# Kernel optimization log

Hardware: AMD Instinct MI355X
Metric: run time of the kernel (lower is better)

## Reference

```python
import jax, jax.numpy as jnp
import numpy as np

GROUP_SIZE = 128
NIBBLES = 8  # int4 values packed per int32


def dequantize(qweight, qzeros, scales):
    """Unpack int4 weights/zeros and dequantize: w = (q - z) * scale.

    qweight: [in/8, out] int32, 8 int4 values packed along the IN dim.
    qzeros:  [groups, out/8] int32, 8 int4 zeros packed along the OUT dim.
    scales:  [groups, out] fp16.
    Returns w: [in, out] fp16.
    """
    shifts = (jnp.arange(NIBBLES, dtype=jnp.int32) * 4)
    # unpack weights along input dim -> [in/8, 8, out] -> [in, out]
    q = ((qweight[:, None, :] >> shifts[None, :, None]) & 15)
    q = q.reshape(-1, qweight.shape[1])
    # unpack zeros along output dim -> [groups, out/8, 8] -> [groups, out]
    z = ((qzeros[:, :, None] >> shifts[None, None, :]) & 15)
    z = z.reshape(qzeros.shape[0], -1)
    # broadcast per-group zeros/scales to per-input-row
    z_full = jnp.repeat(z, GROUP_SIZE, axis=0).astype(scales.dtype)   # [in, out]
    s_full = jnp.repeat(scales, GROUP_SIZE, axis=0)                    # [in, out]
    return (q.astype(scales.dtype) - z_full) * s_full


def setup_inputs() -> dict:
    key = jax.random.key(0)
    k1, k2, k3, k4, k5 = jax.random.split(key, 5)
    B, S, IN, OUT, G = 2, 2048, 4096, 11008, 32
    x = jax.random.normal(k1, (B, S, IN), dtype=jnp.float16)
    qweight = jax.random.randint(k2, (IN // 8, OUT), 0, 2147483647, dtype=jnp.int32)
    qzeros = jax.random.randint(k3, (G, OUT // 8), 0, 2147483647, dtype=jnp.int32)
    scales = jax.random.uniform(k4, (G, OUT), dtype=jnp.float16, minval=0.001, maxval=0.02)
    bias = jax.random.normal(k5, (OUT,), dtype=jnp.float16)
    return {"x": x, "qweight": qweight, "qzeros": qzeros, "scales": scales, "bias": bias}


def reference(x, qweight, qzeros, scales, bias):
    w = dequantize(qweight, qzeros, scales)  # [in, out] fp16
    # q4_matmul accumulates in fp32, emits fp16
    out = jnp.einsum('bsi,io->bso', x, w, preferred_element_type=jnp.float32)
    out = out.astype(jnp.float16) + bias
    return out
```

## Files before the change

kernel.cpp:

```cpp
#include <hip/hip_runtime.h>
#include <cstdint>
#include <cstddef>


typedef unsigned short u16;
typedef u16    u16x8  __attribute__((ext_vector_type(8)));
typedef __bf16 bfv8   __attribute__((ext_vector_type(8)));
typedef float  f32x4  __attribute__((ext_vector_type(4)));

#define K_DIM 4096
#define N_DIM 11008
#define GS    128
#define KT64  (K_DIM / 64)
#define LSTR  72

__device__ __forceinline__ u16 f2bf(float f) {
  union { float f; uint32_t u; } v;
  v.f = f;
  uint32_t u = v.u + 0x7FFFu + ((v.u >> 16) & 1u);
  return (u16)(u >> 16);
}
__device__ __forceinline__ float f16r(float v) {
  return (float)(_Float16)v;
}
__device__ __forceinline__ void async_load16(const u16* g, u16* l) {
  __builtin_amdgcn_global_load_lds(
      (const __attribute__((address_space(1))) uint32_t*)g,
      (__attribute__((address_space(3))) uint32_t*)l, 16, 0, 0);
}

__global__ __launch_bounds__(256) void convert_x_tiled(
    const float* __restrict__ x, u16* __restrict__ xb) {
  const int kt = blockIdx.x, mt = blockIdx.y;
  const int k0 = kt * 64, m0 = mt * 128;
  u16* dst = xb + ((size_t)(mt * KT64 + kt)) * 8192;
#pragma unroll
  for (int i = 0; i < 4; ++i) {
    const int g  = i * 256 + threadIdx.x;
    const int nl = g >> 3;
    const int cg = (g & 7) ^ (nl & 7);
    const float* sp = x + (size_t)(m0 + nl) * K_DIM + (k0 + cg * 8);
    const f32x4 p = *(const f32x4*)sp;
    const f32x4 q = *(const f32x4*)(sp + 4);
    u16x8 o;
#pragma unroll
    for (int t = 0; t < 4; ++t) { o[t] = f2bf(p[t]); o[t + 4] = f2bf(q[t]); }
    *(u16x8*)(dst + (size_t)g * 8) = o;
  }
}

__global__ __launch_bounds__(256) void dequant_tiled(
    const uint32_t* __restrict__ qweight, const uint32_t* __restrict__ qzeros,
    const float* __restrict__ scales, u16* __restrict__ wt) {
  const int kt = blockIdx.x, nt = blockIdx.y;
  const int n0 = nt * 128;
  const int gq = kt >> 1;
  u16* dst = wt + ((size_t)(nt * KT64 + kt)) * 8192;
#pragma unroll
  for (int i = 0; i < 4; ++i) {
    const int g  = i * 256 + threadIdx.x;
    const int nl = g >> 3;
    const int cg = (g & 7) ^ (nl & 7);
    const int n  = n0 + nl;
    const uint32_t zq = qzeros[(size_t)gq * (N_DIM / 8) + (n >> 3)];
    const int   z   = (int)((zq >> ((n & 7) * 4)) & 15u);
    const float s   = scales[(size_t)gq * N_DIM + n];
    const float nzs = -s * (float)z;
    const uint32_t q = qweight[(size_t)(kt * 8 + cg) * N_DIM + n];
    u16x8 o;
#pragma unroll
    for (int t = 0; t < 8; ++t) {
      const int qv = (int)((q >> (t * 4)) & 15u);
      o[t] = f2bf(fmaf((float)qv, s, nzs));
    }
    *(u16x8*)(dst + (size_t)g * 8) = o;
  }
}

#define LDF(p) __builtin_bit_cast(bfv8, *(const u16x8*)(p))
#define BAR()  asm volatile("s_barrier" ::: "memory")
#define VMW(n) asm volatile("s_waitcnt vmcnt(" #n ")" ::: "memory")

#define STAGE_AH(ktt, h) do {                                                 \
    const u16* s_ = at0 + ((size_t)(h) * KT64 + (ktt)) * 8192;                \
    u16* d_ = &As[(((ktt) & 1) * 16384) + (h) * 8192 + wave * 512];           \
    async_load16(s_ + (size_t)tid * 8, d_);                                   \
    async_load16(s_ + (size_t)(512 + tid) * 8, d_ + 4096);                    \
  } while (0)
#define STAGE_BH(ktt, h) do {                                                 \
    const u16* s_ = bt0 + ((size_t)(h) * KT64 + (ktt)) * 8192;                \
    u16* d_ = &Bs[(((ktt) & 1) * 16384) + (h) * 8192 + wave * 512];           \
    async_load16(s_ + (size_t)tid * 8, d_);                                   \
    async_load16(s_ + (size_t)(512 + tid) * 8, d_ + 4096);                    \
  } while (0)

#define RD_AP(v, ib, sbx) do {                                                \
    v[0] = LDF(&As[(sbx) * 16384 + aoff + (ib) * 1024 + kq0]);                \
    v[1] = LDF(&As[(sbx) * 16384 + aoff + (ib) * 1024 + kq1]);                \
    v[2] = LDF(&As[(sbx) * 16384 + aoff + ((ib) + 1) * 1024 + kq0]);          \
    v[3] = LDF(&As[(sbx) * 16384 + aoff + ((ib) + 1) * 1024 + kq1]);          \
  } while (0)
#define RD_B8(v, sbx) do {                                                    \
    _Pragma("unroll")                                                         \
    for (int j_ = 0; j_ < 4; ++j_) {                                          \
      v[2 * j_]     = LDF(&Bs[(sbx) * 16384 + boff + j_ * 1024 + kq0]);       \
      v[2 * j_ + 1] = LDF(&Bs[(sbx) * 16384 + boff + j_ * 1024 + kq1]);       \
    }                                                                         \
  } while (0)

#define MM(ib, av, bv) do {                                                   \
    __builtin_amdgcn_s_setprio(1);                                            \
    _Pragma("unroll")                                                         \
    for (int ks_ = 0; ks_ < 2; ++ks_)                                         \
      _Pragma("unroll")                                                       \
      for (int ii_ = 0; ii_ < 2; ++ii_)                                       \
        _Pragma("unroll")                                                     \
        for (int j_ = 0; j_ < 4; ++j_)                                        \
          acc[(ib) + ii_][j_] = __builtin_amdgcn_mfma_f32_16x16x32_bf16(      \
              av[2 * ii_ + ks_], bv[2 * j_ + ks_], acc[(ib) + ii_][j_],       \
              0, 0, 0);                                                       \
    __builtin_amdgcn_s_setprio(0);                                            \
  } while (0)

#define KTILE_BODY(kt, sb, bcur, bnxt) do {                                   \
    RD_AP(a23, 2, sb);  STAGE_AH((kt) + 1, 0);  MM(0, a01, bcur);  BAR();     \
    RD_AP(a45, 4, sb);  STAGE_AH((kt) + 1, 1);  MM(2, a23, bcur);  BAR();     \
    RD_AP(a67, 6, sb);  STAGE_BH((kt) + 2, 0);  MM(4, a45, bcur);             \
    VMW(2);  BAR();                                                           \
    RD_B8(bnxt, (sb) ^ 1);  RD_AP(a01, 0, (sb) ^ 1);  STAGE_BH((kt) + 2, 1);  \
    MM(6, a67, bcur);  BAR();                                                 \
  } while (0)

__global__ __launch_bounds__(512, 2) void gemm_256(
    const u16* __restrict__ xb, const u16* __restrict__ wt,
    const float* __restrict__ bias, float* __restrict__ out) {
  __shared__ __align__(16) u16 As[2 * 16384];
  __shared__ __align__(16) u16 Bs[2 * 16384];

  const int tid  = threadIdx.x;
  const int lane = tid & 63;
  const int wave = tid >> 6;
  const int wm   = wave >> 2;
  const int wn   = wave & 3;
  const int lrow = lane & 15;
  const int lk   = lane >> 4;
  const int swz  = lrow & 7;

  const int nwg = gridDim.x * gridDim.y;
  int wg = blockIdx.y * gridDim.x + blockIdx.x;
  if ((nwg & 7) == 0) wg = (wg & 7) * (nwg >> 3) + (wg >> 3);
  const int bx = wg % gridDim.x;
  const int by = wg / gridDim.x;
  const int n0 = bx * 256;
  const int m0 = by * 256;

  const u16* at0 = xb + (size_t)(2 * by) * KT64 * 8192;
  const u16* bt0 = wt + (size_t)(2 * bx) * KT64 * 8192;

  const int aoff = wm * 8192 + lrow * 64;
  const int boff = (wn >> 1) * 8192 + ((wn & 1) * 64 + lrow) * 64;
  const int kq0  = (lk ^ swz) * 8;
  const int kq1  = ((4 + lk) ^ swz) * 8;

  bfv8 a01[4], a23[4], a45[4], a67[4], bA[8], bB[8];
  f32x4 acc[8][4];
#pragma unroll
  for (int i = 0; i < 8; ++i)
#pragma unroll
    for (int j = 0; j < 4; ++j) acc[i][j] = f32x4{0.f, 0.f, 0.f, 0.f};

  STAGE_AH(0, 0); STAGE_AH(0, 1); STAGE_BH(0, 0); STAGE_BH(0, 1);
  STAGE_BH(1, 0); STAGE_BH(1, 1);
  VMW(4); BAR();
  RD_B8(bA, 0); RD_AP(a01, 0, 0);

#pragma unroll 1
  for (int kt2 = 0; kt2 < 31; ++kt2) {
    const int kt = 2 * kt2;
    KTILE_BODY(kt,     0, bA, bB);
    KTILE_BODY(kt + 1, 1, bB, bA);
  }
  RD_AP(a23, 2, 0);  STAGE_AH(63, 0);  MM(0, a01, bA);  BAR();
  RD_AP(a45, 4, 0);  STAGE_AH(63, 1);  MM(2, a23, bA);  BAR();
  RD_AP(a67, 6, 0);                    MM(4, a45, bA);  VMW(0); BAR();
  RD_B8(bB, 1); RD_AP(a01, 0, 1);      MM(6, a67, bA);  BAR();
  RD_AP(a23, 2, 1);  MM(0, a01, bB);  BAR();
  RD_AP(a45, 4, 1);  MM(2, a23, bB);  BAR();
  RD_AP(a67, 6, 1);  MM(4, a45, bB);  BAR();
                     MM(6, a67, bB);

#pragma unroll
  for (int j = 0; j < 4; ++j) {
    const int n = n0 + wn * 64 + j * 16 + lrow;
    const float bvf = bias[n];
#pragma unroll
    for (int i = 0; i < 8; ++i) {
      const int mrow = m0 + wm * 128 + i * 16 + lk * 4;
#pragma unroll
      for (int r = 0; r < 4; ++r) {
        out[(size_t)(mrow + r) * N_DIM + n] = f16r(f16r(acc[i][j][r]) + bvf);
      }
    }
  }
}

__global__ __launch_bounds__(256) void gemm_fused(
    const float* __restrict__ xf, const uint32_t* __restrict__ qw,
    const uint32_t* __restrict__ qzeros, const float* __restrict__ scales,
    const float* __restrict__ bias, float* __restrict__ out) {
  __shared__ __align__(16) u16 As[128 * LSTR];
  __shared__ __align__(16) u16 Bs[128 * LSTR];

  const int tid  = threadIdx.x;
  const int lane = tid & 63;
  const int wave = tid >> 6;
  const int n0 = blockIdx.x * 128;
  const int m0 = blockIdx.y * 128;
  const int m_off = (wave >> 1) * 64;
  const int n_off = (wave & 1) * 64;
  const int lrow  = lane & 15;
  const int lk    = lane >> 4;
  const int sm = tid >> 3;
  const int sc = tid & 7;

  f32x4 acc[4][4];
#pragma unroll
  for (int i = 0; i < 4; ++i)
#pragma unroll
    for (int j = 0; j < 4; ++j) acc[i][j] = f32x4{0.f, 0.f, 0.f, 0.f};

  const int ncol = n0 + (tid & 127);
  float s_cur = 0.f, nzs_cur = 0.f;

  for (int kt = 0; kt < K_DIM / 64; ++kt) {
    const int k0 = kt * 64;
    u16x8 av[4];
#pragma unroll
    for (int i = 0; i < 4; ++i) {
      const int m = i * 32 + sm;
      const float* sp = xf + (size_t)(m0 + m) * K_DIM + (k0 + sc * 8);
      const f32x4 p = *(const f32x4*)sp;
      const f32x4 q4 = *(const f32x4*)(sp + 4);
#pragma unroll
      for (int t = 0; t < 4; ++t) { av[i][t] = f2bf(p[t]); av[i][t+4] = f2bf(q4[t]); }
    }
    u16x8 bv[4];
    if ((k0 & (GS - 1)) == 0) {
      const int g = k0 >> 7;
      const uint32_t zq = qzeros[(size_t)g * (N_DIM / 8) + (ncol >> 3)];
      const int z = (int)((zq >> ((ncol & 7) * 4)) & 15u);
      s_cur = scales[(size_t)g * N_DIM + ncol];
      nzs_cur = -s_cur * (float)z;
    }
#pragma unroll
    for (int i = 0; i < 4; ++i) {
      const int k8l = (tid >> 7) + i * 2;
      const uint32_t q = qw[(size_t)(k0 / 8 + k8l) * N_DIM + ncol];
#pragma unroll
      for (int t = 0; t < 8; ++t) {
        const int qv = (int)((q >> (t * 4)) & 15u);
        bv[i][t] = f2bf(fmaf((float)qv, s_cur, nzs_cur));
      }
    }
#pragma unroll
    for (int i = 0; i < 4; ++i)
      *(u16x8*)&As[(i * 32 + sm) * LSTR + sc * 8] = av[i];
    {
      const int nl = tid & 127;
#pragma unroll
      for (int i = 0; i < 4; ++i) {
        const int k8l = (tid >> 7) + i * 2;
        *(u16x8*)&Bs[nl * LSTR + k8l * 8] = bv[i];
      }
    }
    __syncthreads();
#pragma unroll
    for (int ks = 0; ks < 2; ++ks) {
      const int c = (ks * 4 + lk) * 8;
      bfv8 a[4], b[4];
#pragma unroll
      for (int i = 0; i < 4; ++i)
        a[i] = __builtin_bit_cast(bfv8,
                 *(const u16x8*)&As[(m_off + i * 16 + lrow) * LSTR + c]);
#pragma unroll
      for (int j = 0; j < 4; ++j)
        b[j] = __builtin_bit_cast(bfv8,
                 *(const u16x8*)&Bs[(n_off + j * 16 + lrow) * LSTR + c]);
#pragma unroll
      for (int i = 0; i < 4; ++i)
#pragma unroll
        for (int j = 0; j < 4; ++j)
          acc[i][j] = __builtin_amdgcn_mfma_f32_16x16x32_bf16(a[i], b[j],
                                                              acc[i][j], 0, 0, 0);
    }
    __syncthreads();
  }
#pragma unroll
  for (int j = 0; j < 4; ++j) {
    const int n = n0 + n_off + j * 16 + lrow;
    const float bvf = bias[n];
#pragma unroll
    for (int i = 0; i < 4; ++i) {
      const int mrow = m0 + m_off + i * 16 + lk * 4;
#pragma unroll
      for (int r = 0; r < 4; ++r)
        out[(size_t)(mrow + r) * N_DIM + n] = f16r(f16r(acc[i][j][r]) + bvf);
    }
  }
}

extern "C" void kernel_launch(void* const* d_in, const int* in_sizes, int n_in,
                              void* d_out, int out_size, void* d_ws, size_t ws_size,
                              hipStream_t stream) {
  const float* x = nullptr;      const uint32_t* qweight = nullptr;
  const uint32_t* qzeros = nullptr;
  const float* scales = nullptr; const float* bias = nullptr;
  int M = 4096;
  for (int i = 0; i < n_in; ++i) {
    const long long s = in_sizes[i];
    if      (s == (long long)(K_DIM / 8) * N_DIM) qweight = (const uint32_t*)d_in[i];
    else if (s == (long long)(K_DIM / GS) * (N_DIM / 8)) qzeros = (const uint32_t*)d_in[i];
    else if (s == (long long)(K_DIM / GS) * N_DIM) scales = (const float*)d_in[i];
    else if (s == (long long)N_DIM) bias = (const float*)d_in[i];
    else { x = (const float*)d_in[i]; M = (int)(s / K_DIM); }
  }
  float* out = (float*)d_out;

  const size_t xb_bytes = (size_t)M * K_DIM * sizeof(u16);
  const size_t wt_bytes = (size_t)N_DIM * K_DIM * sizeof(u16);

  if (ws_size >= xb_bytes + wt_bytes && (M % 256) == 0) {
    u16* xbp = (u16*)d_ws;
    u16* wtp = (u16*)((char*)d_ws + xb_bytes);
    convert_x_tiled<<<dim3(KT64, M / 128), 256, 0, stream>>>(x, xbp);
    dequant_tiled<<<dim3(KT64, N_DIM / 128), 256, 0, stream>>>(
        qweight, qzeros, scales, wtp);
    gemm_256<<<dim3(N_DIM / 256, M / 256), 512, 0, stream>>>(
        xbp, wtp, bias, out);
  } else {
    gemm_fused<<<dim3(N_DIM / 128, (M + 127) / 128), 256, 0, stream>>>(
        x, qweight, qzeros, scales, bias, out);
  }
}
```

Baseline: 614.3 us.

## Load dequantized weights directly to registers and deepen activation LDS pipeline

The B operand (dequantized weight tiles) is no longer staged through LDS. Each wave loads its B fragments straight from global memory into registers one k-tile ahead, and the dequant kernel's XOR swizzle is dropped so those direct loads see a contiguous layout. The freed LDS turns A staging into a 4-deep ring buffer prefetched three tiles ahead, with fewer barriers per tile. This removes LDS traffic and barriers for B, but adds global-load latency exposure and register pressure at 2 waves/SIMD, and vmcnt waits now cover mixed B and A loads.

```diff
diff --git a/kernel.cpp b/kernel.cpp
--- a/kernel.cpp
+++ b/kernel.cpp
@@ -60,7 +60,7 @@
   for (int i = 0; i < 4; ++i) {
     const int g  = i * 256 + threadIdx.x;
     const int nl = g >> 3;
-    const int cg = (g & 7) ^ (nl & 7);
+    const int cg = g & 7;
     const int n  = n0 + nl;
     const uint32_t zq = qzeros[(size_t)gq * (N_DIM / 8) + (n >> 3)];
     const int   z   = (int)((zq >> ((n & 7) * 4)) & 15u);
@@ -77,19 +77,14 @@
   }
 }
 
-#define LDF(p) __builtin_bit_cast(bfv8, *(const u16x8*)(p))
-#define BAR()  asm volatile("s_barrier" ::: "memory")
-#define VMW(n) asm volatile("s_waitcnt vmcnt(" #n ")" ::: "memory")
+#define LDF(p)  __builtin_bit_cast(bfv8, *(const u16x8*)(p))
+#define BAR()   asm volatile("s_barrier" ::: "memory")
+#define VMW_(n) asm volatile("s_waitcnt vmcnt(" #n ")" ::: "memory")
+#define VMW(n)  VMW_(n)
 
 #define STAGE_AH(ktt, h) do {                                                 \
     const u16* s_ = at0 + ((size_t)(h) * KT64 + (ktt)) * 8192;                \
-    u16* d_ = &As[(((ktt) & 1) * 16384) + (h) * 8192 + wave * 512];           \
-    async_load16(s_ + (size_t)tid * 8, d_);                                   \
-    async_load16(s_ + (size_t)(512 + tid) * 8, d_ + 4096);                    \
-  } while (0)
-#define STAGE_BH(ktt, h) do {                                                 \
-    const u16* s_ = bt0 + ((size_t)(h) * KT64 + (ktt)) * 8192;                \
-    u16* d_ = &Bs[(((ktt) & 1) * 16384) + (h) * 8192 + wave * 512];           \
+    u16* d_ = &As[(((ktt) & 3) * 16384) + (h) * 8192 + wave * 512];           \
     async_load16(s_ + (size_t)tid * 8, d_);                                   \
     async_load16(s_ + (size_t)(512 + tid) * 8, d_ + 4096);                    \
   } while (0)
@@ -100,12 +95,11 @@
     v[2] = LDF(&As[(sbx) * 16384 + aoff + ((ib) + 1) * 1024 + kq0]);          \
     v[3] = LDF(&As[(sbx) * 16384 + aoff + ((ib) + 1) * 1024 + kq1]);          \
   } while (0)
-#define RD_B8(v, sbx) do {                                                    \
-    _Pragma("unroll")                                                         \
-    for (int j_ = 0; j_ < 4; ++j_) {                                          \
-      v[2 * j_]     = LDF(&Bs[(sbx) * 16384 + boff + j_ * 1024 + kq0]);       \
-      v[2 * j_ + 1] = LDF(&Bs[(sbx) * 16384 + boff + j_ * 1024 + kq1]);       \
-    }                                                                         \
+
+#define BLOAD4(dst, ktt, jb) do {                                             \
+    const u16* p_ = gB + (size_t)(ktt) * 8192 + (jb) * 1024;                  \
+    dst[2 * (jb)]     = LDF(p_);        dst[2 * (jb) + 1] = LDF(p_ + 32);     \
+    dst[2 * (jb) + 2] = LDF(p_ + 1024); dst[2 * (jb) + 3] = LDF(p_ + 1056);   \
   } while (0)
 
 #define MM(ib, av, bv) do {                                                   \
@@ -122,20 +116,28 @@
     __builtin_amdgcn_s_setprio(0);                                            \
   } while (0)
 
-#define KTILE_BODY(kt, sb, bcur, bnxt) do {                                   \
-    RD_AP(a23, 2, sb);  STAGE_AH((kt) + 1, 0);  MM(0, a01, bcur);  BAR();     \
-    RD_AP(a45, 4, sb);  STAGE_AH((kt) + 1, 1);  MM(2, a23, bcur);  BAR();     \
-    RD_AP(a67, 6, sb);  STAGE_BH((kt) + 2, 0);  MM(4, a45, bcur);             \
-    VMW(2);  BAR();                                                           \
-    RD_B8(bnxt, (sb) ^ 1);  RD_AP(a01, 0, (sb) ^ 1);  STAGE_BH((kt) + 2, 1);  \
-    MM(6, a67, bcur);  BAR();                                                 \
+#define KTILE(kt, bcur, bnxt, DO_B, DO_ST, NVM) do {                          \
+    const int sb_  = (kt) & 3;                                                \
+    RD_AP(a23, 2, sb_);                                                       \
+    if (DO_B) { BLOAD4(bnxt, (kt) + 1, 0); }                                  \
+    MM(0, a01, bcur);                                                         \
+    RD_AP(a45, 4, sb_);                                                       \
+    if (DO_B) { BLOAD4(bnxt, (kt) + 1, 2); }                                  \
+    MM(2, a23, bcur);                                                         \
+    RD_AP(a67, 6, sb_);                                                       \
+    MM(4, a45, bcur);                                                         \
+    BAR();                                                                    \
+    if (DO_B) { RD_AP(a01, 0, ((kt) + 1) & 3); }                              \
+    if (DO_ST) { STAGE_AH((kt) + 3, 0); STAGE_AH((kt) + 3, 1); }              \
+    MM(6, a67, bcur);                                                         \
+    VMW(NVM);                                                                 \
+    BAR();                                                                    \
   } while (0)
 
 __global__ __launch_bounds__(512, 2) void gemm_256(
     const u16* __restrict__ xb, const u16* __restrict__ wt,
     const float* __restrict__ bias, float* __restrict__ out) {
-  __shared__ __align__(16) u16 As[2 * 16384];
-  __shared__ __align__(16) u16 Bs[2 * 16384];
+  __shared__ __align__(16) u16 As[4 * 16384];
 
   const int tid  = threadIdx.x;
   const int lane = tid & 63;
@@ -155,10 +157,11 @@
   const int m0 = by * 256;
 
   const u16* at0 = xb + (size_t)(2 * by) * KT64 * 8192;
-  const u16* bt0 = wt + (size_t)(2 * bx) * KT64 * 8192;
+
+  const u16* gB = wt + ((size_t)(2 * bx + (wn >> 1)) * KT64) * 8192
+                + ((wn & 1) * 64 + lrow) * 64 + lk * 8;
 
   const int aoff = wm * 8192 + lrow * 64;
-  const int boff = (wn >> 1) * 8192 + ((wn & 1) * 64 + lrow) * 64;
   const int kq0  = (lk ^ swz) * 8;
   const int kq1  = ((4 + lk) ^ swz) * 8;
 
@@ -169,25 +172,23 @@
 #pragma unroll
     for (int j = 0; j < 4; ++j) acc[i][j] = f32x4{0.f, 0.f, 0.f, 0.f};
 
-  STAGE_AH(0, 0); STAGE_AH(0, 1); STAGE_BH(0, 0); STAGE_BH(0, 1);
-  STAGE_BH(1, 0); STAGE_BH(1, 1);
+  BLOAD4(bA, 0, 0); BLOAD4(bA, 0, 2);
+  STAGE_AH(0, 0); STAGE_AH(0, 1);
+  STAGE_AH(1, 0); STAGE_AH(1, 1);
+  STAGE_AH(2, 0); STAGE_AH(2, 1);
   VMW(4); BAR();
-  RD_B8(bA, 0); RD_AP(a01, 0, 0);
+  RD_AP(a01, 0, 0);
 
 #pragma unroll 1
-  for (int kt2 = 0; kt2 < 31; ++kt2) {
+  for (int kt2 = 0; kt2 < 30; ++kt2) {
     const int kt = 2 * kt2;
-    KTILE_BODY(kt,     0, bA, bB);
-    KTILE_BODY(kt + 1, 1, bB, bA);
-  }
-  RD_AP(a23, 2, 0);  STAGE_AH(63, 0);  MM(0, a01, bA);  BAR();
-  RD_AP(a45, 4, 0);  STAGE_AH(63, 1);  MM(2, a23, bA);  BAR();
-  RD_AP(a67, 6, 0);                    MM(4, a45, bA);  VMW(0); BAR();
-  RD_B8(bB, 1); RD_AP(a01, 0, 1);      MM(6, a67, bA);  BAR();
-  RD_AP(a23, 2, 1);  MM(0, a01, bB);  BAR();
-  RD_AP(a45, 4, 1);  MM(2, a23, bB);  BAR();
-  RD_AP(a67, 6, 1);  MM(4, a45, bB);  BAR();
-                     MM(6, a67, bB);
+    KTILE(kt,     bA, bB, 1, 1, 4);
+    KTILE(kt + 1, bB, bA, 1, 1, 4);
+  }
+  KTILE(60, bA, bB, 1, 1, 4);
+  KTILE(61, bB, bA, 1, 0, 0);
+  KTILE(62, bA, bB, 1, 0, 0);
+  KTILE(63, bB, bA, 0, 0, 0);
 
 #pragma unroll
   for (int j = 0; j < 4; ++j) {
```

New measurement: 700.9 us. 14.1% more time.
